# Kernel optimization log

Measured on AMD Instinct MI355X. Metric: run time of the kernel, lower is better.

## Reference

```python
import jax, jax.numpy as jnp
import numpy as np

EMBED_DIM = 128
N_NODES = 100000
N_PAIRS = 500000


def setup_inputs() -> dict:
    key = jax.random.key(0)
    k_h, k_p, k1, k2, k3, kb1, kb2, kb3 = jax.random.split(key, 8)
    h = jax.random.normal(k_h, (N_NODES, EMBED_DIM), dtype=jnp.float32)
    pairs = jax.random.randint(k_p, (N_PAIRS, 2), 0, N_NODES, dtype=jnp.int64)
    d_in = EMBED_DIM * 4  # 512
    # Kaiming-uniform-ish init scales
    W1 = jax.random.normal(k1, (d_in, 128), dtype=jnp.float32) / np.sqrt(d_in)
    b1 = jnp.zeros((128,), dtype=jnp.float32)
    W2 = jax.random.normal(k2, (128, 64), dtype=jnp.float32) / np.sqrt(128)
    b2 = jnp.zeros((64,), dtype=jnp.float32)
    W3 = jax.random.normal(k3, (64, 1), dtype=jnp.float32) / np.sqrt(64)
    b3 = jnp.zeros((1,), dtype=jnp.float32)
    return {"h": h, "pairs": pairs, "W1": W1, "b1": b1, "W2": W2, "b2": b2, "W3": W3, "b3": b3}


def reference(h, pairs, W1, b1, W2, b2, W3, b3):
    # Gather source/target node embeddings
    hs = h[pairs[:, 0]]  # [P, D]
    ht = h[pairs[:, 1]]  # [P, D]
    feat = jnp.concatenate([hs, ht, hs * ht, jnp.abs(hs - ht)], axis=1)  # [P, 4D]
    # 3-layer MLP (dropout is identity in eval mode)
    x = jax.nn.relu(feat @ W1 + b1)
    x = jax.nn.relu(x @ W2 + b2)
    logit = (x @ W3 + b3)[:, 0]  # [P]
    return logit
```

## Files before the change

### kernel.cpp

```cpp
#include <hip/hip_runtime.h>
#include <math.h>

#define EMBED 128
#define NPB 128

typedef short s16x8 __attribute__((ext_vector_type(8)));
typedef float f32x16 __attribute__((ext_vector_type(16)));
#define MF(a, b, c) __builtin_amdgcn_mfma_f32_32x32x16_bf16((a), (b), (c), 0, 0, 0)

__device__ __forceinline__ unsigned short f2bf(float f) {
    unsigned u = __float_as_uint(f);
    return (unsigned short)((u + 0x7FFF + ((u >> 16) & 1)) >> 16);
}
__device__ __forceinline__ float bf2f(unsigned short h) {
    return __uint_as_float(((unsigned)h) << 16);
}

__global__ void detect_kernel(const unsigned int* __restrict__ pairs,
                              int* __restrict__ flag) {
    unsigned v = 0;
    int lane = threadIdx.x;
#pragma unroll
    for (int i = 0; i < 8; ++i) v |= pairs[2 * (lane * 8 + i) + 1];
    unsigned long long b = __ballot(v != 0);
    if (lane == 0) *flag = (b != 0ULL) ? 1 : 0;
}

__global__ __launch_bounds__(256) void setup_w_kernel(
    const float* __restrict__ W1, const float* __restrict__ W2,
    unsigned short* __restrict__ W1Fh, unsigned short* __restrict__ W1Fl,
    unsigned short* __restrict__ W2Fh, unsigned short* __restrict__ W2Fl)
{
    int gid = blockIdx.x * 256 + threadIdx.x;
    if (gid < 8192) {
        int f = gid;
        int jt = f >> 11, r = f & 2047;
        int gk = r >> 6, lane = r & 63;
        int j = jt * 32 + (lane & 31);
        int kb = gk * 16 + (lane >> 5) * 8;
#pragma unroll
        for (int e = 0; e < 8; ++e) {
            float w = W1[(size_t)(kb + e) * 128 + j];
            unsigned short hb = f2bf(w);
            unsigned short lb = f2bf(w - bf2f(hb));
            W1Fh[(size_t)f * 8 + e] = hb;
            W1Fl[(size_t)f * 8 + e] = lb;
        }
    } else if (gid < 9216) {
        int f = gid - 8192;
        int nt = f >> 9, r = f & 511;
        int gk = r >> 6, lane = r & 63;
        int i = nt * 32 + (lane & 31);
        int kb = gk * 16 + (lane >> 5) * 8;
#pragma unroll
        for (int e = 0; e < 8; ++e) {
            float w = W2[(size_t)(kb + e) * 64 + i];
            unsigned short hb = f2bf(w);
            unsigned short lb = f2bf(w - bf2f(hb));
            W2Fh[(size_t)f * 8 + e] = hb;
            W2Fl[(size_t)f * 8 + e] = lb;
        }
    }
}

template<int MODE>
__device__ __forceinline__ void make_frag_r(
    const float4* ha, const float4* hb, int ks, s16x8& aH, s16x8& aL)
{
    float av[8], bv[8];
    {
        float4 a0 = ha[2 * ks], a1 = ha[2 * ks + 1];
        av[0] = a0.x; av[1] = a0.y; av[2] = a0.z; av[3] = a0.w;
        av[4] = a1.x; av[5] = a1.y; av[6] = a1.z; av[7] = a1.w;
        float4 b0 = hb[2 * ks], b1 = hb[2 * ks + 1];
        bv[0] = b0.x; bv[1] = b0.y; bv[2] = b0.z; bv[3] = b0.w;
        bv[4] = b1.x; bv[5] = b1.y; bv[6] = b1.z; bv[7] = b1.w;
    }
#pragma unroll
    for (int e = 0; e < 8; ++e) {
        float v;
        if (MODE == 0)      v = av[e];
        else if (MODE == 1) v = bv[e];
        else if (MODE == 2) v = av[e] * bv[e];
        else                v = fabsf(av[e] - bv[e]);
        unsigned short hbit = f2bf(v);
        unsigned short lbit = f2bf(v - bf2f(hbit));
        aH[e] = (short)hbit; aL[e] = (short)lbit;
    }
}

template<int MODE>
__device__ __forceinline__ void l1_phase_r(
    const float4* ha, const float4* hb,
    const unsigned short* __restrict__ W1Fh, const unsigned short* __restrict__ W1Fl,
    int lane, int gkbase,
    f32x16& ac0, f32x16& ac1, f32x16& ac2, f32x16& ac3)
{
#pragma unroll
    for (int ks = 0; ks < 4; ++ks) {
        s16x8 aH, aL;
        make_frag_r<MODE>(ha, hb, ks, aH, aL);
        int gk = gkbase + ks;
        size_t bi0 = ((size_t)(0 * 32 + gk) * 64 + lane) * 8;
        size_t bi1 = ((size_t)(1 * 32 + gk) * 64 + lane) * 8;
        size_t bi2 = ((size_t)(2 * 32 + gk) * 64 + lane) * 8;
        size_t bi3 = ((size_t)(3 * 32 + gk) * 64 + lane) * 8;
        s16x8 bH0 = *(const s16x8*)&W1Fh[bi0];
        s16x8 bL0 = *(const s16x8*)&W1Fl[bi0];
        s16x8 bH1 = *(const s16x8*)&W1Fh[bi1];
        s16x8 bL1 = *(const s16x8*)&W1Fl[bi1];
        s16x8 bH2 = *(const s16x8*)&W1Fh[bi2];
        s16x8 bL2 = *(const s16x8*)&W1Fl[bi2];
        s16x8 bH3 = *(const s16x8*)&W1Fh[bi3];
        s16x8 bL3 = *(const s16x8*)&W1Fl[bi3];
        ac0 = MF(aH, bH0, ac0); ac0 = MF(aH, bL0, ac0); ac0 = MF(aL, bH0, ac0);
        ac1 = MF(aH, bH1, ac1); ac1 = MF(aH, bL1, ac1); ac1 = MF(aL, bH1, ac1);
        ac2 = MF(aH, bH2, ac2); ac2 = MF(aH, bL2, ac2); ac2 = MF(aL, bH2, ac2);
        ac3 = MF(aH, bH3, ac3); ac3 = MF(aH, bL3, ac3); ac3 = MF(aL, bH3, ac3);
    }
}

__global__ __launch_bounds__(256) void pair_mfma_kernel(
    const float* __restrict__ h,
    const int* __restrict__ pairs,
    const int* __restrict__ flag,
    const unsigned short* __restrict__ W1Fh, const unsigned short* __restrict__ W1Fl,
    const unsigned short* __restrict__ W2Fh, const unsigned short* __restrict__ W2Fl,
    const float* __restrict__ b1, const float* __restrict__ b2,
    const float* __restrict__ W3, const float* __restrict__ b3,
    float* __restrict__ out, int npairs)
{
    __shared__ __align__(16) char buf[69632];
    unsigned short* fbH = (unsigned short*)buf;
    unsigned short* fbL = (unsigned short*)(buf + 34816);

    int tid  = threadIdx.x;
    int lane = tid & 63;
    int w    = tid >> 6;
    int pb   = blockIdx.x * NPB;

    int ghalf = lane >> 5;
    int pA = w * 32 + (lane & 31);

    int p = pb + pA; if (p >= npairs) p = npairs - 1;
    int s, t;
    if (*flag == 0) { s = pairs[4 * p]; t = pairs[4 * p + 2]; }
    else            { s = pairs[2 * p]; t = pairs[2 * p + 1]; }
    const float4* hsP = (const float4*)(h + (size_t)s * EMBED);
    const float4* htP = (const float4*)(h + (size_t)t * EMBED);

    float bj0 = b1[  0 + (lane & 31)];
    float bj1 = b1[ 32 + (lane & 31)];
    float bj2 = b1[ 64 + (lane & 31)];
    float bj3 = b1[ 96 + (lane & 31)];
    f32x16 ac0, ac1, ac2, ac3;
#pragma unroll
    for (int rg = 0; rg < 16; ++rg) { ac0[rg] = bj0; ac1[rg] = bj1; ac2[rg] = bj2; ac3[rg] = bj3; }

    float4 ha[8], hb[8];

#pragma unroll
    for (int ks = 0; ks < 4; ++ks) {
        ha[2 * ks]     = hsP[ks * 4 + ghalf * 2];
        ha[2 * ks + 1] = hsP[ks * 4 + ghalf * 2 + 1];
        hb[2 * ks]     = htP[ks * 4 + ghalf * 2];
        hb[2 * ks + 1] = htP[ks * 4 + ghalf * 2 + 1];
    }
    l1_phase_r<0>(ha, hb, W1Fh, W1Fl, lane,  0, ac0, ac1, ac2, ac3);
    l1_phase_r<1>(ha, hb, W1Fh, W1Fl, lane,  8, ac0, ac1, ac2, ac3);
    l1_phase_r<2>(ha, hb, W1Fh, W1Fl, lane, 16, ac0, ac1, ac2, ac3);
    l1_phase_r<3>(ha, hb, W1Fh, W1Fl, lane, 24, ac0, ac1, ac2, ac3);

#pragma unroll
    for (int ks = 0; ks < 4; ++ks) {
        ha[2 * ks]     = hsP[16 + ks * 4 + ghalf * 2];
        ha[2 * ks + 1] = hsP[16 + ks * 4 + ghalf * 2 + 1];
        hb[2 * ks]     = htP[16 + ks * 4 + ghalf * 2];
        hb[2 * ks + 1] = htP[16 + ks * 4 + ghalf * 2 + 1];
    }
    l1_phase_r<0>(ha, hb, W1Fh, W1Fl, lane,  4, ac0, ac1, ac2, ac3);
    l1_phase_r<1>(ha, hb, W1Fh, W1Fl, lane, 12, ac0, ac1, ac2, ac3);
    l1_phase_r<2>(ha, hb, W1Fh, W1Fl, lane, 20, ac0, ac1, ac2, ac3);
    l1_phase_r<3>(ha, hb, W1Fh, W1Fl, lane, 28, ac0, ac1, ac2, ac3);

#define X1WR(ACC, jt) do {                                                   \
    int jbase = (jt) * 32 + (lane & 31);                                     \
    int gj = jbase >> 3, jrem = jbase & 7;                                   \
    _Pragma("unroll")                                                        \
    for (int reg = 0; reg < 16; ++reg) {                                     \
        int pr = w * 32 + (reg & 3) + 8 * (reg >> 2) + 4 * ghalf;            \
        float x = fmaxf(ACC[reg], 0.0f);                                     \
        unsigned short hbit = f2bf(x);                                       \
        unsigned short lbit = f2bf(x - bf2f(hbit));                          \
        int idx = pr * 136 + ((gj ^ ((pr >> 3) & 7)) * 8) + jrem;            \
        fbH[idx] = hbit; fbL[idx] = lbit;                                    \
    } } while (0)

    X1WR(ac0, 0); X1WR(ac1, 1); X1WR(ac2, 2); X1WR(ac3, 3);
#undef X1WR
    __syncthreads();

    int pB0 = 64 * (w & 1) + (lane & 31), pB1 = pB0 + 32;
    int oB0base = pB0 * 136, oB1base = pB1 * 136;
    int sb0 = (pB0 >> 3) & 7, sb1 = (pB1 >> 3) & 7;
    int nt = w >> 1;
    int iCol = nt * 32 + (lane & 31);

    float b2v = b2[iCol];
    f32x16 c20, c21;
#pragma unroll
    for (int rg = 0; rg < 16; ++rg) { c20[rg] = b2v; c21[rg] = b2v; }

#pragma unroll
    for (int ks = 0; ks < 8; ++ks) {
        int g = ks * 2 + ghalf;
        int o0 = oB0base + (g ^ sb0) * 8;
        int o1 = oB1base + (g ^ sb1) * 8;
        s16x8 aH0 = *(const s16x8*)&fbH[o0];
        s16x8 aL0 = *(const s16x8*)&fbL[o0];
        s16x8 aH1 = *(const s16x8*)&fbH[o1];
        s16x8 aL1 = *(const s16x8*)&fbL[o1];
        size_t bi = ((size_t)(nt * 8 + ks) * 64 + lane) * 8;
        s16x8 bH = *(const s16x8*)&W2Fh[bi];
        s16x8 bL = *(const s16x8*)&W2Fl[bi];
        c20 = MF(aH0, bH, c20); c20 = MF(aH0, bL, c20); c20 = MF(aL0, bH, c20);
        c21 = MF(aH1, bH, c21); c21 = MF(aH1, bL, c21); c21 = MF(aL1, bH, c21);
    }
    __syncthreads();

    float* red = (float*)buf;
    {
        float w3v = W3[iCol];
#pragma unroll
        for (int reg = 0; reg < 16; ++reg) {
            int pr = 64 * (w & 1) + (reg & 3) + 8 * (reg >> 2) + 4 * ghalf;
            red[pr * 68 + iCol] = fmaxf(c20[reg], 0.0f) * w3v;
        }
#pragma unroll
        for (int reg = 0; reg < 16; ++reg) {
            int pr = 64 * (w & 1) + 32 + (reg & 3) + 8 * (reg >> 2) + 4 * ghalf;
            red[pr * 68 + iCol] = fmaxf(c21[reg], 0.0f) * w3v;
        }
    }
    __syncthreads();

    if (tid < NPB) {
        int po = pb + tid;
        if (po < npairs) {
            const float4* r4 = (const float4*)(red + tid * 68);
            float ssum = 0.0f;
#pragma unroll
            for (int q = 0; q < 16; ++q) {
                float4 v = r4[q];
                ssum += v.x + v.y + v.z + v.w;
            }
            out[po] = ssum + b3[0];
        }
    }
}

__global__ __launch_bounds__(256) void mlp_kernel(
    const float* __restrict__ h,
    const int* __restrict__ pairs,
    const int* __restrict__ flag,
    const float* __restrict__ W1, const float* __restrict__ b1,
    const float* __restrict__ W2, const float* __restrict__ b2,
    const float* __restrict__ W3, const float* __restrict__ b3,
    float* __restrict__ out, int npairs)
{
    int p = blockIdx.x * 256 + threadIdx.x;
    if (p >= npairs) return;
    int s, t;
    if (*flag == 0) { s = pairs[4 * p]; t = pairs[4 * p + 2]; }
    else            { s = pairs[2 * p]; t = pairs[2 * p + 1]; }
    const float4* hs4 = (const float4*)(h + (size_t)s * EMBED);
    const float4* ht4 = (const float4*)(h + (size_t)t * EMBED);
    float acc[128];
#pragma unroll
    for (int j = 0; j < 128; ++j) acc[j] = b1[j];
#pragma unroll 1
    for (int d4 = 0; d4 < EMBED / 4; ++d4) {
        float4 a = hs4[d4]; float4 b = ht4[d4];
        float av[4] = {a.x, a.y, a.z, a.w};
        float bv[4] = {b.x, b.y, b.z, b.w};
#pragma unroll
        for (int dd = 0; dd < 4; ++dd) {
            int k = d4 * 4 + dd;
            float f0 = av[dd], f1 = bv[dd];
            float f2 = f0 * f1, f3 = fabsf(f0 - f1);
            const float* w0 = W1 + (size_t)k * 128;
            const float* w1r = w0 + 128 * 128;
            const float* w2r = w0 + 256 * 128;
            const float* w3r = w0 + 384 * 128;
#pragma unroll
            for (int j = 0; j < 128; ++j) {
                float v0 = acc[j];
                v0 = fmaf(f0, w0[j], v0); v0 = fmaf(f1, w1r[j], v0);
                v0 = fmaf(f2, w2r[j], v0); v0 = fmaf(f3, w3r[j], v0);
                acc[j] = v0;
            }
        }
    }
#pragma unroll
    for (int j = 0; j < 128; ++j) acc[j] = fmaxf(acc[j], 0.0f);
    float x2[64];
#pragma unroll
    for (int j = 0; j < 64; ++j) x2[j] = b2[j];
#pragma unroll
    for (int k = 0; k < 128; ++k) {
        float xv = acc[k];
#pragma unroll
        for (int j = 0; j < 64; ++j)
            x2[j] = fmaf(xv, W2[(size_t)k * 64 + j], x2[j]);
    }
    float lg = b3[0];
#pragma unroll
    for (int k = 0; k < 64; ++k)
        lg = fmaf(fmaxf(x2[k], 0.0f), W3[k], lg);
    out[p] = lg;
}

extern "C" void kernel_launch(void* const* d_in, const int* in_sizes, int n_in,
                              void* d_out, int out_size, void* d_ws, size_t ws_size,
                              hipStream_t stream) {
    const float* h   = (const float*)d_in[0];
    const int* pairs = (const int*)d_in[1];
    const float* W1  = (const float*)d_in[2];
    const float* b1  = (const float*)d_in[3];
    const float* W2  = (const float*)d_in[4];
    const float* b2  = (const float*)d_in[5];
    const float* W3  = (const float*)d_in[6];
    const float* b3  = (const float*)d_in[7];
    float* out = (float*)d_out;

    int npairs = out_size;

    int* flag = (int*)d_ws;
    unsigned short* base = (unsigned short*)((char*)d_ws + 16);
    unsigned short* W1Fh = base;
    unsigned short* W1Fl = base + 65536;
    unsigned short* W2Fh = base + 131072;
    unsigned short* W2Fl = base + 139264;
    size_t need = 16 + (size_t)(65536 * 2 + 8192 * 2) * sizeof(unsigned short);

    detect_kernel<<<1, 64, 0, stream>>>((const unsigned int*)pairs, flag);

    if (ws_size >= need) {
        setup_w_kernel<<<36, 256, 0, stream>>>(W1, W2, W1Fh, W1Fl, W2Fh, W2Fl);
        pair_mfma_kernel<<<(npairs + NPB - 1) / NPB, 256, 0, stream>>>(
            h, pairs, flag, W1Fh, W1Fl, W2Fh, W2Fl, b1, b2, W3, b3, out, npairs);
    } else {
        mlp_kernel<<<(npairs + 255) / 256, 256, 0, stream>>>(
            h, pairs, flag, W1, b1, W2, b2, W3, b3, out, npairs);
    }
}
```

Measured before the change: 267.6 us.

## Halve shared staging buffer by processing layer-2 in two row halves

Layer-1 activations are now staged into LDS in two passes of 64 pairs each: waves 0-1 write their split bf16 hi/lo rows, all four waves run layer 2 on that half, then waves 2-3 write theirs and layer 2 runs again. This halves the block's LDS footprint, so more blocks can be resident per CU, which is meant to improve latency hiding for the gather-heavy kernel. The cost is two extra block-wide barriers and serialisation: half the waves sit idle during each staging write, and the layer-2 MFMA work is split into two dependent phases.

```diff
diff --git a/kernel.cpp b/kernel.cpp
--- a/kernel.cpp
+++ b/kernel.cpp
@@ -130,9 +130,9 @@
     const float* __restrict__ W3, const float* __restrict__ b3,
     float* __restrict__ out, int npairs)
 {
-    __shared__ __align__(16) char buf[69632];
+    __shared__ __align__(16) char buf[34816];
     unsigned short* fbH = (unsigned short*)buf;
-    unsigned short* fbL = (unsigned short*)(buf + 34816);
+    unsigned short* fbL = (unsigned short*)(buf + 17408);
 
     int tid  = threadIdx.x;
     int lane = tid & 63;
@@ -188,58 +188,62 @@
     int gj = jbase >> 3, jrem = jbase & 7;                                   \
     _Pragma("unroll")                                                        \
     for (int reg = 0; reg < 16; ++reg) {                                     \
-        int pr = w * 32 + (reg & 3) + 8 * (reg >> 2) + 4 * ghalf;            \
+        int rIdx = (w & 1) * 32 + (reg & 3) + 8 * (reg >> 2) + 4 * ghalf;    \
         float x = fmaxf(ACC[reg], 0.0f);                                     \
         unsigned short hbit = f2bf(x);                                       \
         unsigned short lbit = f2bf(x - bf2f(hbit));                          \
-        int idx = pr * 136 + ((gj ^ ((pr >> 3) & 7)) * 8) + jrem;            \
+        int idx = rIdx * 136 + ((gj ^ ((rIdx >> 3) & 7)) * 8) + jrem;        \
         fbH[idx] = hbit; fbL[idx] = lbit;                                    \
     } } while (0)
 
-    X1WR(ac0, 0); X1WR(ac1, 1); X1WR(ac2, 2); X1WR(ac3, 3);
-#undef X1WR
-    __syncthreads();
-
-    int pB0 = 64 * (w & 1) + (lane & 31), pB1 = pB0 + 32;
-    int oB0base = pB0 * 136, oB1base = pB1 * 136;
-    int sb0 = (pB0 >> 3) & 7, sb1 = (pB1 >> 3) & 7;
+    int pB = (w & 1) * 32 + (lane & 31);
+    int oBbase = pB * 136;
+    int sb = (pB >> 3) & 7;
     int nt = w >> 1;
     int iCol = nt * 32 + (lane & 31);
-
     float b2v = b2[iCol];
+
+#define L2HALF(CC) do {                                                      \
+    _Pragma("unroll")                                                        \
+    for (int ks = 0; ks < 8; ++ks) {                                         \
+        int g = ks * 2 + ghalf;                                              \
+        int o = oBbase + ((g ^ sb) * 8);                                     \
+        s16x8 aH = *(const s16x8*)&fbH[o];                                   \
+        s16x8 aL = *(const s16x8*)&fbL[o];                                   \
+        size_t bi = ((size_t)(nt * 8 + ks) * 64 + lane) * 8;                 \
+        s16x8 bH = *(const s16x8*)&W2Fh[bi];                                 \
+        s16x8 bL = *(const s16x8*)&W2Fl[bi];                                 \
+        CC = MF(aH, bH, CC); CC = MF(aH, bL, CC); CC = MF(aL, bH, CC);       \
+    } } while (0)
+
     f32x16 c20, c21;
 #pragma unroll
     for (int rg = 0; rg < 16; ++rg) { c20[rg] = b2v; c21[rg] = b2v; }
 
-#pragma unroll
-    for (int ks = 0; ks < 8; ++ks) {
-        int g = ks * 2 + ghalf;
-        int o0 = oB0base + (g ^ sb0) * 8;
-        int o1 = oB1base + (g ^ sb1) * 8;
-        s16x8 aH0 = *(const s16x8*)&fbH[o0];
-        s16x8 aL0 = *(const s16x8*)&fbL[o0];
-        s16x8 aH1 = *(const s16x8*)&fbH[o1];
-        s16x8 aL1 = *(const s16x8*)&fbL[o1];
-        size_t bi = ((size_t)(nt * 8 + ks) * 64 + lane) * 8;
-        s16x8 bH = *(const s16x8*)&W2Fh[bi];
-        s16x8 bL = *(const s16x8*)&W2Fl[bi];
-        c20 = MF(aH0, bH, c20); c20 = MF(aH0, bL, c20); c20 = MF(aL0, bH, c20);
-        c21 = MF(aH1, bH, c21); c21 = MF(aH1, bL, c21); c21 = MF(aL1, bH, c21);
-    }
-    __syncthreads();
+    if ((w >> 1) == 0) { X1WR(ac0, 0); X1WR(ac1, 1); X1WR(ac2, 2); X1WR(ac3, 3); }
+    __syncthreads();
+    L2HALF(c20);
+    __syncthreads();
+
+    if ((w >> 1) == 1) { X1WR(ac0, 0); X1WR(ac1, 1); X1WR(ac2, 2); X1WR(ac3, 3); }
+    __syncthreads();
+    L2HALF(c21);
+    __syncthreads();
+#undef X1WR
+#undef L2HALF
 
     float* red = (float*)buf;
     {
         float w3v = W3[iCol];
 #pragma unroll
         for (int reg = 0; reg < 16; ++reg) {
-            int pr = 64 * (w & 1) + (reg & 3) + 8 * (reg >> 2) + 4 * ghalf;
-            red[pr * 68 + iCol] = fmaxf(c20[reg], 0.0f) * w3v;
+            int crow = (reg & 3) + 8 * (reg >> 2) + 4 * ghalf;
+            red[((w & 1) * 32 + crow) * 68 + iCol] = fmaxf(c20[reg], 0.0f) * w3v;
         }
 #pragma unroll
         for (int reg = 0; reg < 16; ++reg) {
-            int pr = 64 * (w & 1) + 32 + (reg & 3) + 8 * (reg >> 2) + 4 * ghalf;
-            red[pr * 68 + iCol] = fmaxf(c21[reg], 0.0f) * w3v;
+            int crow = (reg & 3) + 8 * (reg >> 2) + 4 * ghalf;
+            red[(64 + (w & 1) * 32 + crow) * 68 + iCol] = fmaxf(c21[reg], 0.0f) * w3v;
         }
     }
     __syncthreads();
```

Measured after the change: 558.7 us. 2.09x slower.
